# Optimization experiments

Measured on AMD Instinct MI355X. Metric: run time of the kernel, lower is better.

Reference implementation:

```python
import jax, jax.numpy as jnp
import numpy as np


def setup_inputs() -> dict:
    key = jax.random.key(0)
    ks = jax.random.split(key, 8)
    n_src, n_dst, n_edges = 100000, 50000, 600000
    d_in, d_out = 128, 128
    n_reuse, n_cache = 5000, 8000
    full_dst_len = n_dst + n_reuse

    feat_src = jax.random.normal(ks[0], (n_src, d_in), jnp.float32)
    src = jax.random.randint(ks[1], (n_edges,), 0, n_src)
    dst = jax.random.randint(ks[2], (n_edges,), 0, n_dst)
    # xavier-ish init for the two bias-free Linear layers (stored as [out, in] like torch)
    W_self = jax.random.normal(ks[3], (d_out, d_in), jnp.float32) / np.sqrt(d_in).astype(np.float32)
    W_neigh = jax.random.normal(ks[4], (d_out, d_in), jnp.float32) / np.sqrt(d_in).astype(np.float32)
    # reuse_indices must be unique positions within [0, full_dst_len)
    reuse_indices = jnp.sort(jax.random.permutation(ks[5], full_dst_len)[:n_reuse])
    reuse_embedding = jax.random.normal(ks[6], (n_reuse, d_out), jnp.float32)
    cache_indices = jax.random.randint(ks[7], (n_cache,), 0, full_dst_len)
    return dict(feat_src=feat_src, W_self=W_self, W_neigh=W_neigh,
                reuse_embedding=reuse_embedding, src=src, dst=dst,
                reuse_indices=reuse_indices, cache_indices=cache_indices,
                n_dst=n_dst)


def reference(feat_src, W_self, W_neigh, reuse_embedding, src, dst,
              reuse_indices, cache_indices, n_dst):
    # --- GraphSAGE 'mean' aggregation on a block graph ---
    feat_dst = feat_src[:n_dst]                         # [n_dst, D_in]
    msgs = feat_src[src]                                # [E, D_in] copy_src gather
    ssum = jax.ops.segment_sum(msgs, dst, num_segments=n_dst)          # [n_dst, D_in]
    deg = jax.ops.segment_sum(jnp.ones_like(msgs[:, 0]), dst, num_segments=n_dst)
    h_neigh = jnp.where(deg[:, None] > 0, ssum / jnp.maximum(deg, 1.0)[:, None], 0.0)
    rst = feat_dst @ W_self.T + h_neigh @ W_neigh.T     # fc_self + fc_neigh

    # --- cache-reuse scatter merge (flag == 0 path) ---
    n_reuse = reuse_indices.shape[0]
    full_dst_len = n_dst + n_reuse
    keep = jnp.ones((full_dst_len,), dtype=bool).at[reuse_indices].set(False)
    unprune_indices = jnp.nonzero(keep, size=n_dst)[0]  # np.delete equivalent
    full = jnp.zeros((full_dst_len, rst.shape[1]), rst.dtype)
    full = full.at[unprune_indices].set(rst).at[reuse_indices].set(reuse_embedding)
    cache_embedding = jax.lax.stop_gradient(full[cache_indices])  # .detach()
    return full, cache_embedding
```

## Files before the change

kernel.cpp:

```cpp
#include <hip/hip_runtime.h>

#define N_SRC   100000
#define N_DST   50000
#define D       128
#define MAXDEG  64

#define NB      391
#define CHUNKS  256
#define TOTAL_BLOCKS 2048
#define COUNT_BLOCKS 256

typedef __attribute__((ext_vector_type(8))) short bf16x8;
typedef __attribute__((ext_vector_type(4))) float f32x4;

__device__ __forceinline__ unsigned short f2bf(float f) {
    unsigned u = __float_as_uint(f);
    u += 0x7FFFu + ((u >> 16) & 1u);
    return (unsigned short)(u >> 16);
}
__device__ __forceinline__ float bf2f(unsigned short u) {
    return __uint_as_float((unsigned)u << 16);
}

__global__ __launch_bounds__(256)
void prep_count_kernel(const int* __restrict__ dst,
                       int* __restrict__ cntmat,
                       int n_edges, int cb,
                       const int* __restrict__ reuse_idx,
                       int* __restrict__ rowpos, int n_reuse,
                       const float* __restrict__ Wself,
                       const float* __restrict__ Wneigh,
                       unsigned short* __restrict__ wbf,
                       const float* __restrict__ feat,
                       unsigned int* __restrict__ featbf_u32) {
    __shared__ int lc[NB];
    if (blockIdx.x < COUNT_BLOCKS) {
        for (int i = threadIdx.x; i < NB; i += 256) lc[i] = 0;
        __syncthreads();
        int c = blockIdx.x;
        int e0 = c * cb, e1 = min(n_edges, e0 + cb);
        for (int e = e0 + (int)threadIdx.x; e < e1; e += 256)
            atomicAdd(&lc[dst[e] >> 7], 1);
        __syncthreads();
        for (int i = threadIdx.x; i < NB; i += 256)
            cntmat[c * NB + i] = lc[i];
    } else {
        int stid = (blockIdx.x - COUNT_BLOCKS) * 256 + threadIdx.x;
        const int sstride = (TOTAL_BLOCKS - COUNT_BLOCKS) * 256;

        if (stid < N_DST) {
            int lo = 0, hi = n_reuse;
            while (lo < hi) {
                int mid = (lo + hi) >> 1;
                if (reuse_idx[mid] - mid > stid) hi = mid; else lo = mid + 1;
            }
            rowpos[stid] = stid + lo;
        }
        if (stid < 128 * 256) {
            int n = stid >> 8;
            int k = stid & 255;
            float v = (k < 128) ? Wself[n * 128 + k] : Wneigh[n * 128 + (k - 128)];
            wbf[stid] = f2bf(v);
        }
        const int n4 = N_SRC * (D / 4);
        for (int i = stid; i < n4; i += sstride) {
            float4 v = *(const float4*)(feat + (size_t)i * 4);
            uint2 o;
            o.x = (unsigned)f2bf(v.x) | ((unsigned)f2bf(v.y) << 16);
            o.y = (unsigned)f2bf(v.z) | ((unsigned)f2bf(v.w) << 16);
            *(uint2*)(featbf_u32 + (size_t)i * 2) = o;
        }
    }
}

__global__ __launch_bounds__(256)
void scan_kernel(const int* __restrict__ cntmat,
                 int* __restrict__ offmat,
                 int* __restrict__ bucketbase) {
    __shared__ int bsum[NB];
    __shared__ int bbase[NB + 1];
    int t = threadIdx.x;
    for (int k = t; k < NB; k += 256) {
        int s = 0;
        for (int c = 0; c < CHUNKS; ++c) s += cntmat[c * NB + k];
        bsum[k] = s;
    }
    __syncthreads();
    if (t == 0) {
        int run = 0;
        for (int k = 0; k < NB; ++k) { bbase[k] = run; run += bsum[k]; }
        bbase[NB] = run;
    }
    __syncthreads();
    for (int k = t; k < NB + 1; k += 256) bucketbase[k] = bbase[k];
    for (int k = t; k < NB; k += 256) {
        int run = bbase[k];
        for (int c = 0; c < CHUNKS; ++c) {
            offmat[k * CHUNKS + c] = run;
            run += cntmat[c * NB + k];
        }
    }
}

__global__ __launch_bounds__(256)
void scatter_kernel(const int* __restrict__ src,
                    const int* __restrict__ dst,
                    const int* __restrict__ offmat,
                    uint2* __restrict__ pe,
                    int n_edges, int cb) {
    __shared__ int lc[NB];
    for (int i = threadIdx.x; i < NB; i += 256) lc[i] = 0;
    __syncthreads();
    int c = blockIdx.x;
    int e0 = c * cb, e1 = min(n_edges, e0 + cb);
    for (int e = e0 + (int)threadIdx.x; e < e1; e += 256) {
        int d = dst[e];
        int s = src[e];
        int k = d >> 7;
        int r = atomicAdd(&lc[k], 1);
        int pos = offmat[k * CHUNKS + c] + r;
        pe[pos] = make_uint2((unsigned)s, (unsigned)d);
    }
}

__global__ __launch_bounds__(256)
void fine_ell_kernel(const uint2* __restrict__ pe,
                     const int* __restrict__ bucketbase,
                     int* __restrict__ ell,
                     int* __restrict__ cnt) {
    __shared__ int rc[128];
    int k = blockIdx.x;
    if (threadIdx.x < 128) rc[threadIdx.x] = 0;
    __syncthreads();
    int e0 = bucketbase[k], e1 = bucketbase[k + 1];
    for (int e = e0 + (int)threadIdx.x; e < e1; e += 256) {
        uint2 p = pe[e];
        int d = (int)p.y;
        int slot = atomicAdd(&rc[d & 127], 1);
        if (slot < MAXDEG)
            ell[(size_t)d * MAXDEG + slot] = (int)p.x;
    }
    __syncthreads();
    int row = k * 128 + threadIdx.x;
    if (threadIdx.x < 128 && row < N_DST) cnt[row] = rc[threadIdx.x];
}

__global__ __launch_bounds__(256)
void gather_bf16_kernel(const unsigned short* __restrict__ featbf,
                        const int* __restrict__ ell,
                        const int* __restrict__ cnt,
                        uint4* __restrict__ hneigh_u4) {
    int gid  = blockIdx.x * blockDim.x + threadIdx.x;
    int row  = gid >> 4;
    int lane = gid & 15;
    if (row >= N_DST) return;

    int deg = cnt[row];
    int n = min(deg, MAXDEG);
    float inv = 1.0f / fmaxf((float)deg, 1.0f);
    const int* rell = ell + (size_t)row * MAXDEG;

    float acc[8];
#pragma unroll
    for (int k = 0; k < 8; ++k) acc[k] = 0.f;

    union U { uint4 v; unsigned short us[8]; };
    int j = 0;
    for (; j + 4 <= n; j += 4) {
        int s0 = rell[j + 0];
        int s1 = rell[j + 1];
        int s2 = rell[j + 2];
        int s3 = rell[j + 3];
        U a, b, c, d;
        a.v = *(const uint4*)(featbf + (size_t)s0 * D + lane * 8);
        b.v = *(const uint4*)(featbf + (size_t)s1 * D + lane * 8);
        c.v = *(const uint4*)(featbf + (size_t)s2 * D + lane * 8);
        d.v = *(const uint4*)(featbf + (size_t)s3 * D + lane * 8);
#pragma unroll
        for (int k = 0; k < 8; ++k)
            acc[k] += (bf2f(a.us[k]) + bf2f(b.us[k])) + (bf2f(c.us[k]) + bf2f(d.us[k]));
    }
    for (; j < n; ++j) {
        int s = rell[j];
        U a;
        a.v = *(const uint4*)(featbf + (size_t)s * D + lane * 8);
#pragma unroll
        for (int k = 0; k < 8; ++k) acc[k] += bf2f(a.us[k]);
    }
    uint4 o;
    o.x = (unsigned)f2bf(acc[0] * inv) | ((unsigned)f2bf(acc[1] * inv) << 16);
    o.y = (unsigned)f2bf(acc[2] * inv) | ((unsigned)f2bf(acc[3] * inv) << 16);
    o.z = (unsigned)f2bf(acc[4] * inv) | ((unsigned)f2bf(acc[5] * inv) << 16);
    o.w = (unsigned)f2bf(acc[6] * inv) | ((unsigned)f2bf(acc[7] * inv) << 16);
    hneigh_u4[(size_t)row * 16 + lane] = o;
}

__global__ __launch_bounds__(256, 2)
void gemm_kernel(const unsigned short* __restrict__ featbf,
                 const unsigned short* __restrict__ hneigh,
                 const unsigned short* __restrict__ wbf,
                 const int* __restrict__ rowpos,
                 float* __restrict__ full) {
    __shared__ unsigned short Wl[128 * 256];

    int tid = threadIdx.x;
    {
        int n = tid >> 1;
        int ckbase = (tid & 1) * 16;
        const uint4* s = (const uint4*)(wbf + n * 256);
        uint4* d = (uint4*)(Wl + n * 256);
#pragma unroll
        for (int i = 0; i < 16; ++i) {
            int ck = ckbase + i;
            d[ck ^ (n & 7)] = s[ck];
        }
    }
    __syncthreads();

    int wv   = tid >> 6;
    int lane = tid & 63;
    int l15  = lane & 15;
    int q    = lane >> 4;
    int rowbase = blockIdx.x * 128 + wv * 32;

    f32x4 acc[2][8];
#pragma unroll
    for (int rt = 0; rt < 2; ++rt)
#pragma unroll
        for (int ct = 0; ct < 8; ++ct) acc[rt][ct] = (f32x4){0.f, 0.f, 0.f, 0.f};

    int r0c = min(rowbase + l15,      N_DST - 1);
    int r1c = min(rowbase + 16 + l15, N_DST - 1);

#pragma unroll
    for (int s = 0; s < 8; ++s) {
        const unsigned short* A = (s < 4) ? featbf : hneigh;
        int k0 = (s & 3) * 32 + q * 8;
        bf16x8 a0 = *(const bf16x8*)(A + (size_t)r0c * D + k0);
        bf16x8 a1 = *(const bf16x8*)(A + (size_t)r1c * D + k0);
#pragma unroll
        for (int ct = 0; ct < 8; ++ct) {
            int n = ct * 16 + l15;
            int ck = s * 4 + q;
            bf16x8 b = *(const bf16x8*)(Wl + n * 256 + ((ck ^ (n & 7)) << 3));
            acc[0][ct] = __builtin_amdgcn_mfma_f32_16x16x32_bf16(a0, b, acc[0][ct], 0, 0, 0);
            acc[1][ct] = __builtin_amdgcn_mfma_f32_16x16x32_bf16(a1, b, acc[1][ct], 0, 0, 0);
        }
    }

#pragma unroll
    for (int rt = 0; rt < 2; ++rt) {
#pragma unroll
        for (int reg = 0; reg < 4; ++reg) {
            int gm = rowbase + rt * 16 + q * 4 + reg;
            if (gm < N_DST) {
                int jj = rowpos[gm];
                float* outr = full + (size_t)jj * D + l15;
#pragma unroll
                for (int ct = 0; ct < 8; ++ct)
                    outr[ct * 16] = acc[rt][ct][reg];
            }
        }
    }
}

__global__ __launch_bounds__(256)
void epilogue_kernel(const float* __restrict__ emb,
                     const int* __restrict__ ridx, int n_reuse,
                     float* __restrict__ full,
                     const int* __restrict__ cidx,
                     float* __restrict__ cache_out, int n_cache) {
    int idx = blockIdx.x * blockDim.x + threadIdx.x;
    int row = idx >> 5;
    int c4 = (idx & 31) * 4;
    if (row < n_reuse) {
        *(float4*)&full[(size_t)ridx[row] * D + c4] =
            *(const float4*)&emb[(size_t)row * D + c4];
    } else if (row < n_reuse + n_cache) {
        int r = row - n_reuse;
        int v = cidx[r];
        int lo = 0, hi = n_reuse;
        while (lo < hi) {
            int mid = (lo + hi) >> 1;
            if (ridx[mid] < v) lo = mid + 1; else hi = mid;
        }
        const float* srcp = (lo < n_reuse && ridx[lo] == v)
            ? emb + (size_t)lo * D
            : full + (size_t)v * D;
        *(float4*)&cache_out[(size_t)r * D + c4] = *(const float4*)&srcp[c4];
    }
}

extern "C" void kernel_launch(void* const* d_in, const int* in_sizes, int n_in,
                              void* d_out, int out_size, void* d_ws, size_t ws_size,
                              hipStream_t stream) {
    const float* feat_src  = (const float*)d_in[0];
    const float* W_self    = (const float*)d_in[1];
    const float* W_neigh   = (const float*)d_in[2];
    const float* reuse_emb = (const float*)d_in[3];
    const int*   src       = (const int*)d_in[4];
    const int*   dst       = (const int*)d_in[5];
    const int*   reuse_idx = (const int*)d_in[6];
    const int*   cache_idx = (const int*)d_in[7];

    int n_edges = in_sizes[4];
    int n_reuse = in_sizes[6];
    int n_cache = in_sizes[7];
    int full_len = N_DST + n_reuse;
    int cb = (n_edges + CHUNKS - 1) / CHUNKS;

    float* full = (float*)d_out;
    float* cache_out = full + (size_t)full_len * D;

    size_t hneigh_b = (size_t)N_DST * D * sizeof(unsigned short);
    size_t featbf_b = (size_t)N_SRC * D * sizeof(unsigned short);

    unsigned short* hneigh = (unsigned short*)d_ws;
    unsigned short* featbf = (unsigned short*)((char*)d_ws + hneigh_b);
    int*   cnt    = (int*)((char*)featbf + featbf_b);
    int*   rowpos = cnt + N_DST;
    unsigned short* wbf = (unsigned short*)(rowpos + N_DST);
    int*   cntmat = (int*)(wbf + 128 * 256);
    int*   offmat = cntmat + CHUNKS * NB;
    int*   bucketbase = offmat + NB * CHUNKS;
    uint2* pe = (uint2*)(bucketbase + NB + 2);

    pe = (uint2*)(((size_t)pe + 7) & ~(size_t)7);

    int* ell = (int*)full;

    prep_count_kernel<<<TOTAL_BLOCKS, 256, 0, stream>>>(
        dst, cntmat, n_edges, cb,
        reuse_idx, rowpos, n_reuse, W_self, W_neigh, wbf,
        feat_src, (unsigned int*)featbf);

    scan_kernel<<<1, 256, 0, stream>>>(cntmat, offmat, bucketbase);

    scatter_kernel<<<CHUNKS, 256, 0, stream>>>(
        src, dst, offmat, pe, n_edges, cb);

    fine_ell_kernel<<<NB, 256, 0, stream>>>(pe, bucketbase, ell, cnt);

    gather_bf16_kernel<<<(N_DST * 16 + 255) / 256, 256, 0, stream>>>(
        featbf, ell, cnt, (uint4*)hneigh);

    gemm_kernel<<<(N_DST + 127) / 128, 256, 0, stream>>>(
        featbf, hneigh, wbf, rowpos, full);

    epilogue_kernel<<<((n_reuse + n_cache) * 32 + 255) / 256, 256, 0, stream>>>(
        reuse_emb, reuse_idx, n_reuse, full, cache_idx, cache_out, n_cache);
}
```

Before: 218.3 us.

## Parallelize per-bucket offset scan across blocks with transposed count matrix

The count matrix is now written transposed (bucket-major), so each bucket's chunk counts are contiguous. The single-block serial scan is replaced by a per-bucket parallel Hillis-Steele scan across 391 blocks, followed by a small single-block scan of bucket totals. The scatter kernel adds the bucket base to the relative offset. This removes a long serial, poorly coalesced scan at the cost of one extra kernel launch.

```diff
diff --git a/kernel.cpp b/kernel.cpp
--- a/kernel.cpp
+++ b/kernel.cpp
@@ -24,7 +24,7 @@
 
 __global__ __launch_bounds__(256)
 void prep_count_kernel(const int* __restrict__ dst,
-                       int* __restrict__ cntmat,
+                       int* __restrict__ cntmatT,
                        int n_edges, int cb,
                        const int* __restrict__ reuse_idx,
                        int* __restrict__ rowpos, int n_reuse,
@@ -43,7 +43,7 @@
             atomicAdd(&lc[dst[e] >> 7], 1);
         __syncthreads();
         for (int i = threadIdx.x; i < NB; i += 256)
-            cntmat[c * NB + i] = lc[i];
+            cntmatT[i * CHUNKS + c] = lc[i];
     } else {
         int stid = (blockIdx.x - COUNT_BLOCKS) * 256 + threadIdx.x;
         const int sstride = (TOTAL_BLOCKS - COUNT_BLOCKS) * 256;
@@ -74,38 +74,49 @@
 }
 
 __global__ __launch_bounds__(256)
-void scan_kernel(const int* __restrict__ cntmat,
-                 int* __restrict__ offmat,
-                 int* __restrict__ bucketbase) {
-    __shared__ int bsum[NB];
-    __shared__ int bbase[NB + 1];
+void bucket_scan_kernel(const int* __restrict__ cntmatT,
+                        int* __restrict__ offrel,
+                        int* __restrict__ bsum) {
+    __shared__ int s[CHUNKS];
+    int k = blockIdx.x;
     int t = threadIdx.x;
-    for (int k = t; k < NB; k += 256) {
-        int s = 0;
-        for (int c = 0; c < CHUNKS; ++c) s += cntmat[c * NB + k];
-        bsum[k] = s;
-    }
+    int x = cntmatT[k * CHUNKS + t];
+    s[t] = x;
+    __syncthreads();
+#pragma unroll
+    for (int off = 1; off < CHUNKS; off <<= 1) {
+        int v = (t >= off) ? s[t - off] : 0;
+        __syncthreads();
+        s[t] += v;
+        __syncthreads();
+    }
+    offrel[k * CHUNKS + t] = s[t] - x;
+    if (t == CHUNKS - 1) bsum[k] = s[t];
+}
+
+__global__ __launch_bounds__(256)
+void base_scan_kernel(const int* __restrict__ bsum,
+                      int* __restrict__ bucketbase) {
+    __shared__ int s[NB];
+    __shared__ int tot;
+    int t = threadIdx.x;
+    for (int i = t; i < NB; i += 256) s[i] = bsum[i];
     __syncthreads();
     if (t == 0) {
         int run = 0;
-        for (int k = 0; k < NB; ++k) { bbase[k] = run; run += bsum[k]; }
-        bbase[NB] = run;
-    }
-    __syncthreads();
-    for (int k = t; k < NB + 1; k += 256) bucketbase[k] = bbase[k];
-    for (int k = t; k < NB; k += 256) {
-        int run = bbase[k];
-        for (int c = 0; c < CHUNKS; ++c) {
-            offmat[k * CHUNKS + c] = run;
-            run += cntmat[c * NB + k];
-        }
-    }
+        for (int i = 0; i < NB; ++i) { int v = s[i]; s[i] = run; run += v; }
+        tot = run;
+    }
+    __syncthreads();
+    for (int i = t; i < NB; i += 256) bucketbase[i] = s[i];
+    if (t == 0) bucketbase[NB] = tot;
 }
 
 __global__ __launch_bounds__(256)
 void scatter_kernel(const int* __restrict__ src,
                     const int* __restrict__ dst,
-                    const int* __restrict__ offmat,
+                    const int* __restrict__ offrel,
+                    const int* __restrict__ bucketbase,
                     uint2* __restrict__ pe,
                     int n_edges, int cb) {
     __shared__ int lc[NB];
@@ -118,7 +129,7 @@
         int s = src[e];
         int k = d >> 7;
         int r = atomicAdd(&lc[k], 1);
-        int pos = offmat[k * CHUNKS + c] + r;
+        int pos = bucketbase[k] + offrel[k * CHUNKS + c] + r;
         pe[pos] = make_uint2((unsigned)s, (unsigned)d);
     }
 }
@@ -320,24 +331,26 @@
     int*   cnt    = (int*)((char*)featbf + featbf_b);
     int*   rowpos = cnt + N_DST;
     unsigned short* wbf = (unsigned short*)(rowpos + N_DST);
-    int*   cntmat = (int*)(wbf + 128 * 256);
-    int*   offmat = cntmat + CHUNKS * NB;
-    int*   bucketbase = offmat + NB * CHUNKS;
+    int*   cntmatT = (int*)(wbf + 128 * 256);
+    int*   offrel  = cntmatT + NB * CHUNKS;
+    int*   bsum    = offrel + NB * CHUNKS;
+    int*   bucketbase = bsum + NB;
     uint2* pe = (uint2*)(bucketbase + NB + 2);
-
     pe = (uint2*)(((size_t)pe + 7) & ~(size_t)7);
 
     int* ell = (int*)full;
 
     prep_count_kernel<<<TOTAL_BLOCKS, 256, 0, stream>>>(
-        dst, cntmat, n_edges, cb,
+        dst, cntmatT, n_edges, cb,
         reuse_idx, rowpos, n_reuse, W_self, W_neigh, wbf,
         feat_src, (unsigned int*)featbf);
 
-    scan_kernel<<<1, 256, 0, stream>>>(cntmat, offmat, bucketbase);
+    bucket_scan_kernel<<<NB, 256, 0, stream>>>(cntmatT, offrel, bsum);
+
+    base_scan_kernel<<<1, 256, 0, stream>>>(bsum, bucketbase);
 
     scatter_kernel<<<CHUNKS, 256, 0, stream>>>(
-        src, dst, offmat, pe, n_edges, cb);
+        src, dst, offrel, bucketbase, pe, n_edges, cb);
 
     fine_ell_kernel<<<NB, 256, 0, stream>>>(pe, bucketbase, ell, cnt);
 
```

Result: faster. 187.1 us (-14.3%).
